# Kernel tuning notes

Hardware: AMD Instinct MI355X
Metric: run time of the kernel (lower is better)

## Reference

```python
import jax, jax.numpy as jnp
import numpy as np

K = 3       # kernel_size
STRIDE = 1
PAD = 1


def conv3d(x, w, b):
    # standard Conv3d NCDHW, used to predict per-tap offsets
    y = jax.lax.conv_general_dilated(
        x, w, window_strides=(STRIDE,) * 3, padding=[(PAD, PAD)] * 3,
        dimension_numbers=("NCDHW", "OIDHW", "NCDHW"))
    return y + b[None, :, None, None, None]


def trilinear_sample(xn, pd, ph, pw):
    # xn: (C,D,H,W); pd/ph/pw: (T,Do,Ho,Wo) float voxel coords.
    # Trilinear interpolation with zeros padding (grid_sample semantics).
    C, D, H, W = xn.shape
    d0 = jnp.floor(pd); h0 = jnp.floor(ph); w0 = jnp.floor(pw)
    fd = pd - d0; fh = ph - h0; fw = pw - w0
    d0 = d0.astype(jnp.int32); h0 = h0.astype(jnp.int32); w0 = w0.astype(jnp.int32)
    out = jnp.zeros((C,) + pd.shape, xn.dtype)
    for dd in (0, 1):
        wd = fd if dd else 1.0 - fd
        di = d0 + dd
        for hh in (0, 1):
            wh = fh if hh else 1.0 - fh
            hi = h0 + hh
            for ww in (0, 1):
                wc = fw if ww else 1.0 - fw
                wi = w0 + ww
                valid = (di >= 0) & (di < D) & (hi >= 0) & (hi < H) & (wi >= 0) & (wi < W)
                wgt = jnp.where(valid, wd * wh * wc, 0.0)
                g = xn[:, jnp.clip(di, 0, D - 1), jnp.clip(hi, 0, H - 1), jnp.clip(wi, 0, W - 1)]
                out = out + wgt[None] * g
    return out  # (C,T,Do,Ho,Wo)


def deform_conv3d(x, offset, weight):
    # x: (N,C,D,H,W); offset: (N,3*K^3,Do,Ho,Wo); weight: (O,C,K,K,K)
    N, C, D, H, W = x.shape
    Do = (D + 2 * PAD - K) // STRIDE + 1
    Ho = (H + 2 * PAD - K) // STRIDE + 1
    Wo = (W + 2 * PAD - K) // STRIDE + 1
    T = K ** 3
    kd, kh, kw = jnp.meshgrid(jnp.arange(K), jnp.arange(K), jnp.arange(K), indexing="ij")
    kd = kd.reshape(T, 1, 1, 1).astype(x.dtype)
    kh = kh.reshape(T, 1, 1, 1).astype(x.dtype)
    kw = kw.reshape(T, 1, 1, 1).astype(x.dtype)
    base_d = kd - PAD + (jnp.arange(Do, dtype=x.dtype) * STRIDE).reshape(1, Do, 1, 1)
    base_h = kh - PAD + (jnp.arange(Ho, dtype=x.dtype) * STRIDE).reshape(1, 1, Ho, 1)
    base_w = kw - PAD + (jnp.arange(Wo, dtype=x.dtype) * STRIDE).reshape(1, 1, 1, Wo)
    off = offset.reshape(N, 3, T, Do, Ho, Wo)  # matches offset.view(N,3,K,K,K,...) tap ordering
    pd = base_d[None] + off[:, 0]
    ph = base_h[None] + off[:, 1]
    pw = base_w[None] + off[:, 2]
    sampled = jax.vmap(trilinear_sample)(x, pd, ph, pw)  # (N,C,T,Do,Ho,Wo)
    O = weight.shape[0]
    w2 = weight.reshape(O, C, T)
    return jnp.einsum("nctdhw,oct->nodhw", sampled, w2)


def setup_inputs() -> dict:
    key = jax.random.key(0)
    k1, k2, k3 = jax.random.split(key, 3)
    N, C, O, S = 2, 16, 32, 48
    x = jax.random.normal(k1, (N, C, S, S, S), jnp.float32)
    fan_in = C * K ** 3
    weight = jax.random.normal(k2, (O, C, K, K, K), jnp.float32) * (1.0 / np.sqrt(fan_in))
    # offset conv params; small scale so sampled positions stay near the base grid
    offset_w = jax.random.normal(k3, (3 * K ** 3, C, K, K, K), jnp.float32) * 0.02
    offset_b = jnp.zeros((3 * K ** 3,), jnp.float32)
    return {"x": x, "weight": weight, "offset_w": offset_w, "offset_b": offset_b}


def reference(x, weight, offset_w, offset_b):
    offset = conv3d(x, offset_w, offset_b)
    return deform_conv3d(x, offset, weight)
```

## Files before the change

### kernel.cpp

```cpp
#include <hip/hip_runtime.h>
#include <hip/hip_bf16.h>

#define SDIM 48
#define SP   110592
#define C_IN 16
#define O_OUT 32
#define T27  27
#define G81  81

typedef __attribute__((ext_vector_type(8))) short bf16x8;
typedef __attribute__((ext_vector_type(4))) float f32x4;

__device__ __forceinline__ float bf2f(unsigned short u) {
    unsigned int x = ((unsigned int)u) << 16;
    return __builtin_bit_cast(float, x);
}
__device__ __forceinline__ unsigned short f2bf(float f) {
    unsigned int x = __builtin_bit_cast(unsigned int, f);
    x += 0x7fffu + ((x >> 16) & 1u);
    return (unsigned short)(x >> 16);
}

__global__ __launch_bounds__(256)
void prep_xT(const float* __restrict__ x, unsigned short* __restrict__ xT) {
    __shared__ float l[256 * 17];
    const int tid = threadIdx.x;
    const int b   = blockIdx.x;
    const int n   = b / 432;
    const int sp0 = (b - n * 432) * 256;
    #pragma unroll
    for (int c = 0; c < 16; ++c)
        l[tid * 17 + c] = x[((size_t)(n * 16 + c)) * SP + sp0 + tid];
    __syncthreads();
    unsigned int u[8];
    #pragma unroll
    for (int q = 0; q < 8; ++q) {
        unsigned short a = f2bf(l[tid * 17 + 2 * q]);
        unsigned short bb = f2bf(l[tid * 17 + 2 * q + 1]);
        u[q] = (unsigned int)a | ((unsigned int)bb << 16);
    }
    uint4* dst = (uint4*)(xT + ((size_t)(n * SP + sp0 + tid)) * 16);
    dst[0] = make_uint4(u[0], u[1], u[2], u[3]);
    dst[1] = make_uint4(u[4], u[5], u[6], u[7]);
}

__global__ __launch_bounds__(256)
void prep_bfrag(const float* __restrict__ ow, unsigned short* __restrict__ Bf) {
    int idx = blockIdx.x * 256 + threadIdx.x;
    int r    = idx & 7;
    int lane = (idx >> 3) & 63;
    int snt  = idx >> 9;
    int s = snt / 6, nt = snt - s * 6;
    int kk  = ((lane >> 4) << 3) + r;
    int g   = nt * 16 + (lane & 15);
    int tap = 2 * s + (kk >> 4);
    int c   = kk & 15;
    float v = 0.f;
    if (tap < 27 && g < 81) v = ow[((size_t)(g * 16 + c)) * 27 + tap];
    Bf[idx] = f2bf(v);
}

__global__ __launch_bounds__(256)
void prep_wfrag(const float* __restrict__ w, unsigned short* __restrict__ Wf) {
    int idx = blockIdx.x * 256 + threadIdx.x;
    int r    = idx & 7;
    int lane = (idx >> 3) & 63;
    int snt  = idx >> 9;
    int s = snt >> 1, nt = snt & 1;
    int kk  = ((lane >> 4) << 3) + r;
    int o   = nt * 16 + (lane & 15);
    int tap = 2 * s + (kk >> 4);
    int c   = kk & 15;
    float v = 0.f;
    if (tap < 27) v = w[((size_t)(o * 16 + c)) * 27 + tap];
    Wf[idx] = f2bf(v);
}

__global__ __launch_bounds__(256)
void offs_conv_mfma(const unsigned short* __restrict__ xT,
                    const unsigned short* __restrict__ Bf,
                    const float* __restrict__ ob,
                    unsigned short* __restrict__ offs) {
    __shared__ unsigned short Alds[256 * 8];
    const int tid  = threadIdx.x;
    const int lane = tid & 63;
    const int wid  = tid >> 6;
    const int j    = wid;
    const int m    = tid & 63;
    const int gm   = blockIdx.x * 64 + m;
    const int n    = (gm >= SP) ? 1 : 0;
    const int sp   = gm - n * SP;
    const int z    = sp / 2304;
    const int rem  = sp - z * 2304;
    const int y    = rem / 48;
    const int xx   = rem - y * 48;
    const int tapoff = j >> 1;
    const int half   = j & 1;

    auto stage_load = [&](int s) -> uint4 {
        int tap = 2 * s + tapoff;
        int kd = tap / 9;
        int t2 = tap - kd * 9;
        int kh = t2 / 3;
        int kw = t2 - kh * 3;
        int di = z + kd - 1, hi = y + kh - 1, wi = xx + kw - 1;
        bool ok = (tap < 27) && ((unsigned)di < 48u) && ((unsigned)hi < 48u) &&
                  ((unsigned)wi < 48u);
        uint4 v = make_uint4(0u, 0u, 0u, 0u);
        if (ok) {
            size_t off = ((size_t)(n * SP + (di * 2304 + hi * 48 + wi))) * 16 + half * 8;
            v = *(const uint4*)(xT + off);
        }
        return v;
    };

    f32x4 acc[6];
    #pragma unroll
    for (int t = 0; t < 6; ++t) acc[t] = (f32x4){0.f, 0.f, 0.f, 0.f};

    uint4 v = stage_load(0);
    for (int s = 0; s < 14; ++s) {
        __syncthreads();
        *(uint4*)&Alds[tid * 8] = v;
        __syncthreads();
        if (s < 13) v = stage_load(s + 1);
        bf16x8 a = *(const bf16x8*)&Alds[(((lane >> 4) * 64) + (wid * 16) + (lane & 15)) * 8];
        const bf16x8* bp = (const bf16x8*)Bf + (size_t)(s * 6) * 64 + lane;
        #pragma unroll
        for (int nt = 0; nt < 6; ++nt) {
            bf16x8 b = bp[nt * 64];
            acc[nt] = __builtin_amdgcn_mfma_f32_16x16x32_bf16(a, b, acc[nt], 0, 0, 0);
        }
    }

    const int mrow = wid * 16 + ((lane >> 4) << 2);
    const int gmr  = blockIdx.x * 64 + mrow;
    const int n2   = (gmr >= SP) ? 1 : 0;
    const int spr  = gmr - n2 * SP;
    #pragma unroll
    for (int nt = 0; nt < 6; ++nt) {
        int g = nt * 16 + (lane & 15);
        if (g < 81) {
            float bia = ob[g];
            unsigned short h0 = f2bf(acc[nt][0] + bia);
            unsigned short h1 = f2bf(acc[nt][1] + bia);
            unsigned short h2 = f2bf(acc[nt][2] + bia);
            unsigned short h3 = f2bf(acc[nt][3] + bia);
            uint2 pv;
            pv.x = (unsigned int)h0 | ((unsigned int)h1 << 16);
            pv.y = (unsigned int)h2 | ((unsigned int)h3 << 16);
            *(uint2*)(offs + ((size_t)(n2 * 81 + g)) * SP + spr) = pv;
        }
    }
}

__global__ __launch_bounds__(256, 4)
void deform_mfma(const unsigned short* __restrict__ xT,
                 const unsigned short* __restrict__ Wf,
                 const unsigned short* __restrict__ offs,
                 float* __restrict__ out) {
    __shared__ unsigned short Alds[256 * 8];
    __shared__ float olds[32 * 65];
    const int tid  = threadIdx.x;
    const int lane = tid & 63;
    const int wid  = tid >> 6;
    const int j    = wid;
    const int m    = lane;
    const int n    = (blockIdx.x >= 1728) ? 1 : 0;
    const int sp0  = blockIdx.x * 64 - n * SP;
    const int sp   = sp0 + m;
    const int z    = sp / 2304;
    const int rm   = sp - z * 2304;
    const int y    = rm / 48;
    const int xx   = rm - y * 48;
    const int tapoff = j >> 1;
    const int half   = j & 1;

    const unsigned short* offn = offs + (size_t)n * G81 * SP + sp;
    const unsigned short* xb   = xT + (size_t)n * SP * 16;

    auto stage = [&](int s) -> uint4 {
        int tap = 2 * s + tapoff;
        uint4 res = make_uint4(0u, 0u, 0u, 0u);
        if (tap < 27) {
            int kd = tap / 9;
            int t2 = tap - kd * 9;
            int kh = t2 / 3;
            int kw = t2 - kh * 3;
            float pd = (float)(z + kd - 1)  + bf2f(offn[(size_t)tap * SP]);
            float ph = (float)(y + kh - 1)  + bf2f(offn[(size_t)(27 + tap) * SP]);
            float pw = (float)(xx + kw - 1) + bf2f(offn[(size_t)(54 + tap) * SP]);
            float d0f = floorf(pd), h0f = floorf(ph), w0f = floorf(pw);
            float fd = pd - d0f, fh = ph - h0f, fw = pw - w0f;
            int d0 = (int)d0f, h0 = (int)h0f, w0 = (int)w0f;

            float cw[8];
            const uint4* cp[8];
            #pragma unroll
            for (int jj = 0; jj < 8; ++jj) {
                int dd = jj >> 2, hh = (jj >> 1) & 1, ww = jj & 1;
                int di = d0 + dd, hi = h0 + hh, wi = w0 + ww;
                bool ok = ((unsigned)di < 48u) & ((unsigned)hi < 48u) & ((unsigned)wi < 48u);
                float wgt = (dd ? fd : 1.f - fd) * (hh ? fh : 1.f - fh) * (ww ? fw : 1.f - fw);
                cw[jj] = ok ? wgt : 0.f;
                int dc = min(max(di, 0), 47);
                int hc = min(max(hi, 0), 47);
                int wc = min(max(wi, 0), 47);
                cp[jj] = (const uint4*)(xb + ((size_t)((dc * 48 + hc) * 48 + wc)) * 16 + half * 8);
            }
            uint4 cv[8];
            #pragma unroll
            for (int jj = 0; jj < 8; ++jj) cv[jj] = *cp[jj];

            float sm[8];
            #pragma unroll
            for (int q = 0; q < 8; ++q) sm[q] = 0.f;
            #pragma unroll
            for (int jj = 0; jj < 8; ++jj) {
                float wgt = cw[jj];
                unsigned int uu[4] = {cv[jj].x, cv[jj].y, cv[jj].z, cv[jj].w};
                #pragma unroll
                for (int q = 0; q < 4; ++q) {
                    float lo = __builtin_bit_cast(float, uu[q] << 16);
                    float hf = __builtin_bit_cast(float, uu[q] & 0xffff0000u);
                    sm[2 * q]     = fmaf(wgt, lo, sm[2 * q]);
                    sm[2 * q + 1] = fmaf(wgt, hf, sm[2 * q + 1]);
                }
            }
            res.x = (unsigned int)f2bf(sm[0]) | ((unsigned int)f2bf(sm[1]) << 16);
            res.y = (unsigned int)f2bf(sm[2]) | ((unsigned int)f2bf(sm[3]) << 16);
            res.z = (unsigned int)f2bf(sm[4]) | ((unsigned int)f2bf(sm[5]) << 16);
            res.w = (unsigned int)f2bf(sm[6]) | ((unsigned int)f2bf(sm[7]) << 16);
        }
        return res;
    };

    f32x4 acc[2];
    acc[0] = (f32x4){0.f, 0.f, 0.f, 0.f};
    acc[1] = (f32x4){0.f, 0.f, 0.f, 0.f};

    uint4 v = stage(0);
    for (int s = 0; s < 14; ++s) {
        __syncthreads();
        *(uint4*)&Alds[tid * 8] = v;
        __syncthreads();
        if (s < 13) v = stage(s + 1);
        bf16x8 a = *(const bf16x8*)&Alds[(((lane >> 4) * 64) + (wid * 16) + (lane & 15)) * 8];
        const bf16x8* bp = (const bf16x8*)Wf + (size_t)(s * 2) * 64 + lane;
        acc[0] = __builtin_amdgcn_mfma_f32_16x16x32_bf16(a, bp[0],  acc[0], 0, 0, 0);
        acc[1] = __builtin_amdgcn_mfma_f32_16x16x32_bf16(a, bp[64], acc[1], 0, 0, 0);
    }

    __syncthreads();
    const int mr = wid * 16 + ((lane >> 4) << 2);
    #pragma unroll
    for (int nt = 0; nt < 2; ++nt) {
        int o = nt * 16 + (lane & 15);
        #pragma unroll
        for (int r = 0; r < 4; ++r)
            olds[o * 65 + mr + r] = acc[nt][r];
    }
    __syncthreads();
    const int o  = tid >> 3;
    const int m8 = (tid & 7) * 8;
    float* op = out + ((size_t)(n * O_OUT + o)) * SP + sp0 + m8;
    float4 a0 = make_float4(olds[o * 65 + m8],     olds[o * 65 + m8 + 1],
                            olds[o * 65 + m8 + 2], olds[o * 65 + m8 + 3]);
    float4 a1 = make_float4(olds[o * 65 + m8 + 4], olds[o * 65 + m8 + 5],
                            olds[o * 65 + m8 + 6], olds[o * 65 + m8 + 7]);
    *(float4*)op       = a0;
    *(float4*)(op + 4) = a1;
}

extern "C" void kernel_launch(void* const* d_in, const int* in_sizes, int n_in,
                              void* d_out, int out_size, void* d_ws, size_t ws_size,
                              hipStream_t stream) {
    (void)in_sizes; (void)n_in; (void)out_size; (void)ws_size;
    const float* x      = (const float*)d_in[0];
    const float* weight = (const float*)d_in[1];
    const float* ow     = (const float*)d_in[2];
    const float* ob     = (const float*)d_in[3];
    float* out = (float*)d_out;

    unsigned short* offs_b = (unsigned short*)d_ws;
    unsigned short* xT     = offs_b + (size_t)2 * 81 * SP;
    unsigned short* Bf     = xT + (size_t)2 * SP * 16;
    unsigned short* Wf     = Bf + 43008;

    prep_xT<<<864, 256, 0, stream>>>(x, xT);
    prep_bfrag<<<168, 256, 0, stream>>>(ow, Bf);
    prep_wfrag<<<56, 256, 0, stream>>>(weight, Wf);
    offs_conv_mfma<<<3456, 256, 0, stream>>>(xT, Bf, ob, offs_b);
    deform_mfma<<<3456, 256, 0, stream>>>(xT, Wf, offs_b, out);
}
```

Baseline: 183.2 us.

## Assign one tap per wave with all 16 channels per thread in deform sampling

Each wave now handles a whole tap and each thread samples all 16 channels, instead of two waves splitting the channels of one tap. The offset loads, floor math and weight computation are therefore done once per tap and position rather than twice. The main loop drops from 14 steps to 7, with two MFMAs per accumulator per step, and a padded LDS layout (24 shorts per row) is used for the A tiles. Interpolation uses packed 2-wide FMAs and v_cvt_pk_bf16_f32. The cost is more registers per thread (16 uint4 corner loads per stage), which may hurt occupancy under the launch bound of 4 blocks.

```diff
diff --git a/kernel.cpp b/kernel.cpp
--- a/kernel.cpp
+++ b/kernel.cpp
@@ -10,6 +10,7 @@
 
 typedef __attribute__((ext_vector_type(8))) short bf16x8;
 typedef __attribute__((ext_vector_type(4))) float f32x4;
+typedef __attribute__((ext_vector_type(2))) float f32x2;
 
 __device__ __forceinline__ float bf2f(unsigned short u) {
     unsigned int x = ((unsigned int)u) << 16;
@@ -159,12 +160,11 @@
                  const unsigned short* __restrict__ Wf,
                  const unsigned short* __restrict__ offs,
                  float* __restrict__ out) {
-    __shared__ unsigned short Alds[256 * 8];
+    __shared__ unsigned short Alds[4 * 64 * 24];
     __shared__ float olds[32 * 65];
     const int tid  = threadIdx.x;
     const int lane = tid & 63;
     const int wid  = tid >> 6;
-    const int j    = wid;
     const int m    = lane;
     const int n    = (blockIdx.x >= 1728) ? 1 : 0;
     const int sp0  = blockIdx.x * 64 - n * SP;
@@ -173,103 +173,142 @@
     const int rm   = sp - z * 2304;
     const int y    = rm / 48;
     const int xx   = rm - y * 48;
-    const int tapoff = j >> 1;
-    const int half   = j & 1;
 
     const unsigned short* offn = offs + (size_t)n * G81 * SP + sp;
-    const unsigned short* xb   = xT + (size_t)n * SP * 16;
-
-    auto stage = [&](int s) -> uint4 {
-        int tap = 2 * s + tapoff;
-        uint4 res = make_uint4(0u, 0u, 0u, 0u);
-        if (tap < 27) {
-            int kd = tap / 9;
-            int t2 = tap - kd * 9;
-            int kh = t2 / 3;
-            int kw = t2 - kh * 3;
-            float pd = (float)(z + kd - 1)  + bf2f(offn[(size_t)tap * SP]);
-            float ph = (float)(y + kh - 1)  + bf2f(offn[(size_t)(27 + tap) * SP]);
-            float pw = (float)(xx + kw - 1) + bf2f(offn[(size_t)(54 + tap) * SP]);
-            float d0f = floorf(pd), h0f = floorf(ph), w0f = floorf(pw);
-            float fd = pd - d0f, fh = ph - h0f, fw = pw - w0f;
-            int d0 = (int)d0f, h0 = (int)h0f, w0 = (int)w0f;
-
-            float cw[8];
-            const uint4* cp[8];
+    const uint4* xq4 = (const uint4*)(xT + (size_t)n * SP * 16);
+
+    struct Stg { uint4 a, b; };
+
+    auto stage = [&](int rr) -> Stg {
+        Stg res;
+        res.a = make_uint4(0u, 0u, 0u, 0u);
+        res.b = make_uint4(0u, 0u, 0u, 0u);
+        const int tap = 4 * rr + wid;
+        if (tap >= 27) return res;
+        const int kd = tap / 9;
+        const int t2 = tap - kd * 9;
+        const int kh = t2 / 3;
+        const int kw = t2 - kh * 3;
+        float pd = (float)(z + kd - 1)  + bf2f(offn[(size_t)tap * SP]);
+        float ph = (float)(y + kh - 1)  + bf2f(offn[(size_t)(27 + tap) * SP]);
+        float pw = (float)(xx + kw - 1) + bf2f(offn[(size_t)(54 + tap) * SP]);
+        float df = floorf(pd), hf = floorf(ph), wf = floorf(pw);
+        float fd = pd - df, fh = ph - hf, fw = pw - wf;
+        int d0 = (int)df, h0 = (int)hf, w0 = (int)wf;
+        float wd0 = ((unsigned)d0       < 48u) ? (1.f - fd) : 0.f;
+        float wd1 = ((unsigned)(d0 + 1) < 48u) ? fd : 0.f;
+        float wh0 = ((unsigned)h0       < 48u) ? (1.f - fh) : 0.f;
+        float wh1 = ((unsigned)(h0 + 1) < 48u) ? fh : 0.f;
+        float ww0 = ((unsigned)w0       < 48u) ? (1.f - fw) : 0.f;
+        float ww1 = ((unsigned)(w0 + 1) < 48u) ? fw : 0.f;
+        int dc0 = min(max(d0,     0), 47) * 2304;
+        int dc1 = min(max(d0 + 1, 0), 47) * 2304;
+        int hc0 = min(max(h0,     0), 47) * 48;
+        int hc1 = min(max(h0 + 1, 0), 47) * 48;
+        int wc0 = min(max(w0,     0), 47);
+        int wc1 = min(max(w0 + 1, 0), 47);
+
+        float wdh[4] = {wd0 * wh0, wd0 * wh1, wd1 * wh0, wd1 * wh1};
+        int   rdh[4] = {dc0 + hc0, dc0 + hc1, dc1 + hc0, dc1 + hc1};
+
+        f32x2 s2v[8];
+        #pragma unroll
+        for (int q = 0; q < 8; ++q) s2v[q] = (f32x2){0.f, 0.f};
+
+        #pragma unroll
+        for (int g2 = 0; g2 < 2; ++g2) {
+            uint4 cv[8];
+            float cwt[4];
             #pragma unroll
-            for (int jj = 0; jj < 8; ++jj) {
-                int dd = jj >> 2, hh = (jj >> 1) & 1, ww = jj & 1;
-                int di = d0 + dd, hi = h0 + hh, wi = w0 + ww;
-                bool ok = ((unsigned)di < 48u) & ((unsigned)hi < 48u) & ((unsigned)wi < 48u);
-                float wgt = (dd ? fd : 1.f - fd) * (hh ? fh : 1.f - fh) * (ww ? fw : 1.f - fw);
-                cw[jj] = ok ? wgt : 0.f;
-                int dc = min(max(di, 0), 47);
-                int hc = min(max(hi, 0), 47);
-                int wc = min(max(wi, 0), 47);
-                cp[jj] = (const uint4*)(xb + ((size_t)((dc * 48 + hc) * 48 + wc)) * 16 + half * 8);
+            for (int pidx = 0; pidx < 2; ++pidx) {
+                int jj = g2 * 2 + pidx;
+                int i0 = rdh[jj] + wc0;
+                int i1 = rdh[jj] + wc1;
+                cv[pidx * 4 + 0] = xq4[(size_t)i0 * 2];
+                cv[pidx * 4 + 1] = xq4[(size_t)i0 * 2 + 1];
+                cv[pidx * 4 + 2] = xq4[(size_t)i1 * 2];
+                cv[pidx * 4 + 3] = xq4[(size_t)i1 * 2 + 1];
+                cwt[pidx * 2 + 0] = wdh[jj] * ww0;
+                cwt[pidx * 2 + 1] = wdh[jj] * ww1;
             }
-            uint4 cv[8];
             #pragma unroll
-            for (int jj = 0; jj < 8; ++jj) cv[jj] = *cp[jj];
-
-            float sm[8];
-            #pragma unroll
-            for (int q = 0; q < 8; ++q) sm[q] = 0.f;
-            #pragma unroll
-            for (int jj = 0; jj < 8; ++jj) {
-                float wgt = cw[jj];
-                unsigned int uu[4] = {cv[jj].x, cv[jj].y, cv[jj].z, cv[jj].w};
+            for (int pidx = 0; pidx < 2; ++pidx) {
                 #pragma unroll
-                for (int q = 0; q < 4; ++q) {
-                    float lo = __builtin_bit_cast(float, uu[q] << 16);
-                    float hf = __builtin_bit_cast(float, uu[q] & 0xffff0000u);
-                    sm[2 * q]     = fmaf(wgt, lo, sm[2 * q]);
-                    sm[2 * q + 1] = fmaf(wgt, hf, sm[2 * q + 1]);
+                for (int wsel = 0; wsel < 2; ++wsel) {
+                    f32x2 w2;
+                    w2.x = cwt[pidx * 2 + wsel];
+                    w2.y = w2.x;
+                    const uint4& lo4 = cv[pidx * 4 + wsel * 2];
+                    const uint4& hi4 = cv[pidx * 4 + wsel * 2 + 1];
+                    unsigned int wd_[8] = {lo4.x, lo4.y, lo4.z, lo4.w,
+                                           hi4.x, hi4.y, hi4.z, hi4.w};
+                    #pragma unroll
+                    for (int q = 0; q < 8; ++q) {
+                        f32x2 xv;
+                        xv.x = __builtin_bit_cast(float, wd_[q] << 16);
+                        xv.y = __builtin_bit_cast(float, wd_[q] & 0xffff0000u);
+                        s2v[q] = __builtin_elementwise_fma(xv, w2, s2v[q]);
+                    }
                 }
             }
-            res.x = (unsigned int)f2bf(sm[0]) | ((unsigned int)f2bf(sm[1]) << 16);
-            res.y = (unsigned int)f2bf(sm[2]) | ((unsigned int)f2bf(sm[3]) << 16);
-            res.z = (unsigned int)f2bf(sm[4]) | ((unsigned int)f2bf(sm[5]) << 16);
-            res.w = (unsigned int)f2bf(sm[6]) | ((unsigned int)f2bf(sm[7]) << 16);
-        }
+        }
+        unsigned int o_[8];
+        #pragma unroll
+        for (int q = 0; q < 8; ++q) {
+            unsigned int r_;
+            asm("v_cvt_pk_bf16_f32 %0, %1, %2" : "=v"(r_) : "v"(s2v[q].x), "v"(s2v[q].y));
+            o_[q] = r_;
+        }
+        res.a = make_uint4(o_[0], o_[1], o_[2], o_[3]);
+        res.b = make_uint4(o_[4], o_[5], o_[6], o_[7]);
         return res;
     };
 
-    f32x4 acc[2];
-    acc[0] = (f32x4){0.f, 0.f, 0.f, 0.f};
-    acc[1] = (f32x4){0.f, 0.f, 0.f, 0.f};
-
-    uint4 v = stage(0);
-    for (int s = 0; s < 14; ++s) {
+    f32x4 acc0 = (f32x4){0.f, 0.f, 0.f, 0.f};
+    f32x4 acc1 = (f32x4){0.f, 0.f, 0.f, 0.f};
+
+    const int q_   = lane >> 4;
+    const int tl   = q_ >> 1;
+    const int chh  = q_ & 1;
+    const int rowm = wid * 16 + (lane & 15);
+
+    Stg v = stage(0);
+    for (int rr = 0; rr < 7; ++rr) {
         __syncthreads();
-        *(uint4*)&Alds[tid * 8] = v;
+        unsigned short* wp_ = &Alds[(wid * 64 + m) * 24];
+        *(uint4*)wp_ = v.a;
+        *(uint4*)(wp_ + 8) = v.b;
         __syncthreads();
-        if (s < 13) v = stage(s + 1);
-        bf16x8 a = *(const bf16x8*)&Alds[(((lane >> 4) * 64) + (wid * 16) + (lane & 15)) * 8];
-        const bf16x8* bp = (const bf16x8*)Wf + (size_t)(s * 2) * 64 + lane;
-        acc[0] = __builtin_amdgcn_mfma_f32_16x16x32_bf16(a, bp[0],  acc[0], 0, 0, 0);
-        acc[1] = __builtin_amdgcn_mfma_f32_16x16x32_bf16(a, bp[64], acc[1], 0, 0, 0);
+        if (rr < 6) v = stage(rr + 1);
+        bf16x8 a0 = *(const bf16x8*)&Alds[((tl * 64) + rowm) * 24 + chh * 8];
+        bf16x8 a1 = *(const bf16x8*)&Alds[(((2 + tl) * 64) + rowm) * 24 + chh * 8];
+        const bf16x8* bp0 = (const bf16x8*)Wf + (size_t)((2 * rr + 0) * 2) * 64 + lane;
+        const bf16x8* bp1 = (const bf16x8*)Wf + (size_t)((2 * rr + 1) * 2) * 64 + lane;
+        acc0 = __builtin_amdgcn_mfma_f32_16x16x32_bf16(a0, bp0[0],  acc0, 0, 0, 0);
+        acc1 = __builtin_amdgcn_mfma_f32_16x16x32_bf16(a0, bp0[64], acc1, 0, 0, 0);
+        acc0 = __builtin_amdgcn_mfma_f32_16x16x32_bf16(a1, bp1[0],  acc0, 0, 0, 0);
+        acc1 = __builtin_amdgcn_mfma_f32_16x16x32_bf16(a1, bp1[64], acc1, 0, 0, 0);
     }
 
     __syncthreads();
     const int mr = wid * 16 + ((lane >> 4) << 2);
-    #pragma unroll
-    for (int nt = 0; nt < 2; ++nt) {
-        int o = nt * 16 + (lane & 15);
-        #pragma unroll
-        for (int r = 0; r < 4; ++r)
-            olds[o * 65 + mr + r] = acc[nt][r];
+    {
+        int o = lane & 15;
+        #pragma unroll
+        for (int r = 0; r < 4; ++r) olds[o * 65 + mr + r] = acc0[r];
+        #pragma unroll
+        for (int r = 0; r < 4; ++r) olds[(16 + o) * 65 + mr + r] = acc1[r];
     }
     __syncthreads();
     const int o  = tid >> 3;
     const int m8 = (tid & 7) * 8;
     float* op = out + ((size_t)(n * O_OUT + o)) * SP + sp0 + m8;
-    float4 a0 = make_float4(olds[o * 65 + m8],     olds[o * 65 + m8 + 1],
-                            olds[o * 65 + m8 + 2], olds[o * 65 + m8 + 3]);
-    float4 a1 = make_float4(olds[o * 65 + m8 + 4], olds[o * 65 + m8 + 5],
-                            olds[o * 65 + m8 + 6], olds[o * 65 + m8 + 7]);
-    *(float4*)op       = a0;
-    *(float4*)(op + 4) = a1;
+    float4 a0s = make_float4(olds[o * 65 + m8],     olds[o * 65 + m8 + 1],
+                             olds[o * 65 + m8 + 2], olds[o * 65 + m8 + 3]);
+    float4 a1s = make_float4(olds[o * 65 + m8 + 4], olds[o * 65 + m8 + 5],
+                             olds[o * 65 + m8 + 6], olds[o * 65 + m8 + 7]);
+    *(float4*)op       = a0s;
+    *(float4*)(op + 4) = a1s;
 }
 
 extern "C" void kernel_launch(void* const* d_in, const int* in_sizes, int n_in,
```

Result: faster. 171.8 us (-6.2%).
